# Optimization experiments

Measured on AMD Instinct MI355X. Metric: run time of the kernel, lower is better.

The kernel has to match this reference:

```python
import jax, jax.numpy as jnp
import numpy as np

HEADS = 8
DIM_HEAD = 64

def setup_inputs() -> dict:
    key = jax.random.key(0)
    ks = jax.random.split(key, 5)
    B, n, dim = 128, 512, 256
    inner = HEADS * DIM_HEAD  # 512
    return {
        'x': jax.random.normal(ks[0], (B, n, dim), dtype=jnp.float32),
        'Wq': jax.random.normal(ks[1], (dim, inner), dtype=jnp.float32) * (dim ** -0.5),
        'Wkv': jax.random.normal(ks[2], (dim, 2 * inner), dtype=jnp.float32) * (dim ** -0.5),
        'Wo': jax.random.normal(ks[3], (inner, dim), dtype=jnp.float32) * (inner ** -0.5),
        'bo': jnp.zeros((dim,), dtype=jnp.float32),
        'tie_attn_dim': 64,
    }

def reference(x, Wq, Wkv, Wo, bo, tie_attn_dim):
    h, dh = HEADS, DIM_HEAD
    B, n, dim = x.shape
    r = tie_attn_dim
    b = B // r
    q = x @ Wq                      # [B, n, h*dh]
    kv = x @ Wkv                    # [B, n, 2*h*dh] (self-attention: context = x)
    k, v = jnp.split(kv, 2, axis=-1)
    # '(b r) n (h d) -> b r h n d'
    def to_tied(t):
        return t.reshape(b, r, n, h, dh).transpose(0, 1, 3, 2, 4)
    q, k, v = map(to_tied, (q, k, v))
    scale = (dh ** -0.5) * (r ** -0.5)
    # tied row attention: reduce over MSA rows r and head dim d
    dots = jnp.einsum('brhid,brhjd->bhij', q, k) * scale  # [b, h, n, n]
    attn = jax.nn.softmax(dots, axis=-1)
    out = jnp.einsum('bhij,brhjd->brhid', attn, v)        # [b, r, h, n, dh]
    # 'b r h n d -> (b r) n (h d)'
    out = out.transpose(0, 1, 3, 2, 4).reshape(B, n, h * dh)
    return out @ Wo + bo
```

## Files before the change

kernel.cpp:

```cpp
#include <hip/hip_runtime.h>

typedef unsigned short u16;
typedef __attribute__((ext_vector_type(8))) short bf16x8;
typedef __attribute__((ext_vector_type(4))) float f32x4;

struct __align__(8) U16x4 { u16 a, b, c, d; };

__device__ __forceinline__ u16 f2bf(float f) {
  union { float f; unsigned int u; } cv; cv.f = f;
  unsigned int u = cv.u;
  unsigned int r = (u + 0x7fffu + ((u >> 16) & 1u)) >> 16;
  return (u16)r;
}

__device__ __forceinline__ void gld16(const u16* g, u16* l) {
  __builtin_amdgcn_global_load_lds((const __attribute__((address_space(1))) void*)g,
                                   (__attribute__((address_space(3))) void*)l, 16, 0, 0);
}

__global__ void conv_k(const float* __restrict__ x, u16* __restrict__ xbf) {
  size_t i = ((size_t)blockIdx.x * 256 + threadIdx.x) * 8;
  u16 tmp[8];
  #pragma unroll
  for (int j = 0; j < 8; j++) tmp[j] = f2bf(x[i + j]);
  *(bf16x8*)&xbf[i] = *(const bf16x8*)&tmp[0];
}

__global__ void prep_k(const float* __restrict__ Wq, const float* __restrict__ Wkv,
                       const float* __restrict__ Wo, u16* __restrict__ WT1,
                       u16* __restrict__ WoT) {
  int idx = blockIdx.x * 256 + threadIdx.x;
  if (idx < 1536 * 256) {
    int c = idx >> 8, k = idx & 255;
    WT1[idx] = (c < 512) ? f2bf(Wq[(size_t)k * 512 + c])
                         : f2bf(Wkv[(size_t)k * 1024 + (c - 512)]);
  }
  if (idx < 256 * 512) {
    int nn = idx >> 9, kk = idx & 511;
    WoT[idx] = f2bf(Wo[(size_t)kk * 256 + nn]);
  }
}

template<int KIND>
__global__ void __launch_bounds__(256, 2) gemm_k(
    const u16* __restrict__ A, const u16* __restrict__ B,
    u16* __restrict__ C, u16* __restrict__ C2,
    float* __restrict__ SF, const float* __restrict__ bias, int nkRt) {
  __shared__ __align__(16) u16 lA[128 * 32];
  __shared__ __align__(16) u16 lB[128 * 32];

  const int tid  = threadIdx.x;
  const int bid  = blockIdx.x;
  const int lane = tid & 63;
  const int wv   = tid >> 6;
  const int l15  = lane & 15;
  const int quad = lane >> 4;
  const int mq   = (wv & 1) * 64;
  const int nq   = (wv >> 1) * 64;

  int m0, n0, NK, kb0 = 0;
  int r4 = 0, i0 = 0, s = 0, p = 0;
  if constexpr (KIND == 1) {
    m0 = (bid % 256) * 128; n0 = (bid / 256) * 128; NK = 8;
  } else if constexpr (KIND == 2) {
    n0 = (bid & 3) * 128; m0 = ((bid >> 2) & 3) * 128;
    p = (bid >> 4) & 7; s = bid >> 7; NK = nkRt; kb0 = s * nkRt;
  } else if constexpr (KIND == 3) {
    n0 = (bid & 31) * 128; m0 = ((bid >> 5) & 3) * 128; p = bid >> 7; NK = 16;
  } else {
    n0 = (bid & 1) * 128; m0 = (bid >> 1) * 128; NK = 16;
    r4 = (m0 >> 9) & 63; i0 = m0 & 511;
  }

  f32x4 acc[4][4];
  #pragma unroll
  for (int i = 0; i < 4; i++)
    #pragma unroll
    for (int j = 0; j < 4; j++)
      #pragma unroll
      for (int g = 0; g < 4; g++) acc[i][j][g] = 0.f;

  const int ar0 = tid >> 2;
  const int ac0 = (tid & 3) * 8;

  for (int t = 0; t < NK; t++) {
    const int kb = kb0 + t;
    size_t aBase, bBase; int aRS, bRS;
    if constexpr (KIND == 1) {
      aBase = (size_t)m0 * 256 + kb * 32; aRS = 256;
      bBase = (size_t)n0 * 256 + kb * 32; bRS = 256;
    } else if constexpr (KIND == 2) {
      int r = kb >> 1, dlo = (kb & 1) * 32;
      size_t rowblk = (size_t)r * 512;
      aBase = (rowblk + m0) * 1024 + p * 64 + dlo;        aRS = 1024;
      bBase = (rowblk + n0) * 1024 + 512 + p * 64 + dlo;  bRS = 1024;
    } else if constexpr (KIND == 3) {
      aBase = ((size_t)p * 512 + m0) * 512 + kb * 32;   aRS = 512;
      bBase = ((size_t)p * 4096 + n0) * 512 + kb * 32;  bRS = 512;
    } else {
      int h = kb >> 1, dlo = (kb & 1) * 32;
      aBase = ((size_t)h * 512 + i0) * 4096 + r4 * 64 + dlo; aRS = 4096;
      bBase = (size_t)n0 * 512 + kb * 32; bRS = 512;
    }
    gld16(A + aBase + (size_t)ar0 * aRS + ac0,        &lA[tid * 8]);
    gld16(A + aBase + (size_t)(ar0 + 64) * aRS + ac0, &lA[(tid + 256) * 8]);
    gld16(B + bBase + (size_t)ar0 * bRS + ac0,        &lB[tid * 8]);
    gld16(B + bBase + (size_t)(ar0 + 64) * bRS + ac0, &lB[(tid + 256) * 8]);
    __syncthreads();

    bf16x8 af[4], bfr[4];
    #pragma unroll
    for (int mi = 0; mi < 4; mi++)
      af[mi] = *(const bf16x8*)&lA[(mq + mi * 16 + l15) * 32 + quad * 8];
    #pragma unroll
    for (int ni = 0; ni < 4; ni++)
      bfr[ni] = *(const bf16x8*)&lB[(nq + ni * 16 + l15) * 32 + quad * 8];
    #pragma unroll
    for (int mi = 0; mi < 4; mi++)
      #pragma unroll
      for (int ni = 0; ni < 4; ni++)
        acc[mi][ni] = __builtin_amdgcn_mfma_f32_16x16x32_bf16(af[mi], bfr[ni], acc[mi][ni], 0, 0, 0);
    __syncthreads();
  }

  #pragma unroll
  for (int mi = 0; mi < 4; mi++) {
    #pragma unroll
    for (int ni = 0; ni < 4; ni++) {
      if constexpr (KIND == 1) {
        int cgl = n0 + nq + ni * 16 + l15;
        if (n0 < 1024) {
          #pragma unroll
          for (int g = 0; g < 4; g++) {
            int m = m0 + mq + mi * 16 + quad * 4 + g;
            C[(size_t)m * 1024 + cgl] = f2bf(acc[mi][ni][g]);
          }
        } else {
          int cc = cgl - 1024; int h = cc >> 6, d = cc & 63;
          int r = (m0 >> 9) & 63;
          int j0 = (m0 & 511) + mq + mi * 16 + quad * 4;
          U16x4 pk;
          pk.a = f2bf(acc[mi][ni][0]); pk.b = f2bf(acc[mi][ni][1]);
          pk.c = f2bf(acc[mi][ni][2]); pk.d = f2bf(acc[mi][ni][3]);
          *(U16x4*)&C2[((size_t)h * 4096 + r * 64 + d) * 512 + j0] = pk;
        }
      } else if constexpr (KIND == 2) {
        int gn = n0 + nq + ni * 16 + l15;
        #pragma unroll
        for (int g = 0; g < 4; g++) {
          int gm = m0 + mq + mi * 16 + quad * 4 + g;
          SF[((size_t)(s * 8 + p) * 512 + gm) * 512 + gn] = acc[mi][ni][g];
        }
      } else if constexpr (KIND == 3) {
        int gn = n0 + nq + ni * 16 + l15;
        #pragma unroll
        for (int g = 0; g < 4; g++) {
          int gm = m0 + mq + mi * 16 + quad * 4 + g;
          C[((size_t)p * 512 + gm) * 4096 + gn] = f2bf(acc[mi][ni][g]);
        }
      } else {
        int gn = n0 + nq + ni * 16 + l15;
        float bo_f = bias[gn];
        #pragma unroll
        for (int g = 0; g < 4; g++) {
          int gm = m0 + mq + mi * 16 + quad * 4 + g;
          SF[(size_t)gm * 256 + gn] = acc[mi][ni][g] + bo_f;
        }
      }
    }
  }
}

__global__ void softmax_k(const float* __restrict__ SP, u16* __restrict__ P, int nsplit) {
  int bid = blockIdx.x;
  int p = bid >> 9, i = bid & 511;
  int t = threadIdx.x;
  size_t rowbase = ((size_t)p * 512 + i) * 512;
  float v0 = 0.f, v1 = 0.f;
  for (int ss = 0; ss < nsplit; ss++) {
    size_t off = (size_t)ss * 8 * 512 * 512;
    v0 += SP[off + rowbase + t];
    v1 += SP[off + rowbase + t + 256];
  }
  const float scale = 1.0f / 64.0f;
  v0 *= scale; v1 *= scale;

  int wv = t >> 6, ln = t & 63;
  float m = fmaxf(v0, v1);
  for (int o = 32; o > 0; o >>= 1) m = fmaxf(m, __shfl_down(m, o));
  __shared__ float sred[4];
  if (ln == 0) sred[wv] = m;
  __syncthreads();
  m = fmaxf(fmaxf(sred[0], sred[1]), fmaxf(sred[2], sred[3]));

  float e0 = expf(v0 - m), e1 = expf(v1 - m);
  float sum = e0 + e1;
  for (int o = 32; o > 0; o >>= 1) sum += __shfl_down(sum, o);
  __shared__ float sred2[4];
  if (ln == 0) sred2[wv] = sum;
  __syncthreads();
  float inv = 1.0f / (sred2[0] + sred2[1] + sred2[2] + sred2[3]);

  P[rowbase + t]       = f2bf(e0 * inv);
  P[rowbase + t + 256] = f2bf(e1 * inv);
}

extern "C" void kernel_launch(void* const* d_in, const int* in_sizes, int n_in,
                              void* d_out, int out_size, void* d_ws, size_t ws_size,
                              hipStream_t stream) {
  (void)in_sizes; (void)n_in; (void)out_size;
  const float* x   = (const float*)d_in[0];
  const float* Wq  = (const float*)d_in[1];
  const float* Wkv = (const float*)d_in[2];
  const float* Wo  = (const float*)d_in[3];
  const float* bo  = (const float*)d_in[4];
  float* out = (float*)d_out;

  char* ws = (char*)d_ws;
  size_t off = 0;
  u16* WT1 = (u16*)(ws + off); off += (size_t)1536 * 256 * 2;
  u16* WoT = (u16*)(ws + off); off += (size_t)256 * 512 * 2;
  u16* QKb = (u16*)(ws + off); off += (size_t)32768 * 1024 * 2;
  u16* OTb = QKb;
  u16* VTb = (u16*)(ws + off); off += (size_t)8 * 4096 * 512 * 2;
  u16* Pb  = (u16*)(ws + off); off += (size_t)8 * 512 * 512 * 2;
  char* XS = ws + off;
  u16* xbf = (u16*)XS;
  float* SPb = (float*)XS;
  size_t rem = (ws_size > off) ? (ws_size - off) : 0;
  int nsplit = 4;
  while (nsplit > 1 && (size_t)nsplit * 8 * 512 * 512 * 4 > rem) nsplit >>= 1;

  prep_k<<<dim3(1536), dim3(256), 0, stream>>>(Wq, Wkv, Wo, WT1, WoT);

  for (int bt = 0; bt < 2; bt++) {
    const float* xb = x + (size_t)bt * 32768 * 256;
    float* outb = out + (size_t)bt * 32768 * 256;
    conv_k<<<dim3(4096), dim3(256), 0, stream>>>(xb, xbf);
    gemm_k<1><<<dim3(3072), dim3(256), 0, stream>>>(xbf, WT1, QKb, VTb, nullptr, nullptr, 0);
    gemm_k<2><<<dim3(nsplit * 128), dim3(256), 0, stream>>>(QKb, QKb, nullptr, nullptr,
                                                            SPb, nullptr, 128 / nsplit);
    softmax_k<<<dim3(4096), dim3(256), 0, stream>>>(SPb, Pb, nsplit);
    gemm_k<3><<<dim3(1024), dim3(256), 0, stream>>>(Pb, VTb, OTb, nullptr, nullptr, nullptr, 0);
    gemm_k<4><<<dim3(512), dim3(256), 0, stream>>>(OTb, WoT, nullptr, nullptr, outb, bo, 0);
  }
}
```

Baseline: 407.3 us.

## Stage GEMM epilogues through shared memory for coalesced vectorized global stores

New measurement: 415.4 us. 1.02x slower.

```diff
diff --git a/kernel.cpp b/kernel.cpp
--- a/kernel.cpp
+++ b/kernel.cpp
@@ -46,8 +46,9 @@
     const u16* __restrict__ A, const u16* __restrict__ B,
     u16* __restrict__ C, u16* __restrict__ C2,
     float* __restrict__ SF, const float* __restrict__ bias, int nkRt) {
-  __shared__ __align__(16) u16 lA[128 * 32];
-  __shared__ __align__(16) u16 lB[128 * 32];
+  __shared__ __align__(16) u16 lsm[9216];
+  u16* lA = lsm;
+  u16* lB = lsm + 4096;
 
   const int tid  = threadIdx.x;
   const int bid  = blockIdx.x;
@@ -59,7 +60,7 @@
   const int nq   = (wv >> 1) * 64;
 
   int m0, n0, NK, kb0 = 0;
-  int r4 = 0, i0 = 0, s = 0, p = 0;
+  int s = 0, p = 0;
   if constexpr (KIND == 1) {
     m0 = (bid % 256) * 128; n0 = (bid / 256) * 128; NK = 8;
   } else if constexpr (KIND == 2) {
@@ -69,7 +70,6 @@
     n0 = (bid & 31) * 128; m0 = ((bid >> 5) & 3) * 128; p = bid >> 7; NK = 16;
   } else {
     n0 = (bid & 1) * 128; m0 = (bid >> 1) * 128; NK = 16;
-    r4 = (m0 >> 9) & 63; i0 = m0 & 511;
   }
 
   f32x4 acc[4][4];
@@ -99,7 +99,8 @@
       bBase = ((size_t)p * 4096 + n0) * 512 + kb * 32;  bRS = 512;
     } else {
       int h = kb >> 1, dlo = (kb & 1) * 32;
-      aBase = ((size_t)h * 512 + i0) * 4096 + r4 * 64 + dlo; aRS = 4096;
+      aBase = ((size_t)h * 512 + (m0 & 511)) * 4096 + ((m0 >> 9) & 63) * 64 + dlo;
+      aRS = 4096;
       bBase = (size_t)n0 * 512 + kb * 32; bRS = 512;
     }
     gld16(A + aBase + (size_t)ar0 * aRS + ac0,        &lA[tid * 8]);
@@ -123,50 +124,102 @@
     __syncthreads();
   }
 
-  #pragma unroll
-  for (int mi = 0; mi < 4; mi++) {
-    #pragma unroll
-    for (int ni = 0; ni < 4; ni++) {
-      if constexpr (KIND == 1) {
-        int cgl = n0 + nq + ni * 16 + l15;
-        if (n0 < 1024) {
+  if constexpr (KIND == 1 || KIND == 3) {
+    if (KIND == 3 || n0 < 1024) {
+      #pragma unroll
+      for (int ps = 0; ps < 2; ps++) {
+        if ((mq >> 6) == ps) {
           #pragma unroll
-          for (int g = 0; g < 4; g++) {
-            int m = m0 + mq + mi * 16 + quad * 4 + g;
-            C[(size_t)m * 1024 + cgl] = f2bf(acc[mi][ni][g]);
+          for (int mi = 0; mi < 4; mi++)
+            #pragma unroll
+            for (int ni = 0; ni < 4; ni++) {
+              int lr = mi * 16 + quad * 4;
+              int lc = nq + ni * 16 + l15;
+              #pragma unroll
+              for (int g = 0; g < 4; g++)
+                lsm[(lr + g) * 136 + lc] = f2bf(acc[mi][ni][g]);
+            }
+        }
+        __syncthreads();
+        #pragma unroll
+        for (int it = 0; it < 4; it++) {
+          int idx = tid + it * 256;
+          int lr = idx >> 4, c = (idx & 15) * 8;
+          int gm = m0 + ps * 64 + lr;
+          size_t gaddr;
+          if constexpr (KIND == 1) gaddr = (size_t)gm * 1024 + n0 + c;
+          else                     gaddr = ((size_t)p * 512 + gm) * 4096 + n0 + c;
+          *(bf16x8*)&C[gaddr] = *(const bf16x8*)&lsm[lr * 136 + c];
+        }
+        __syncthreads();
+      }
+    } else {
+      #pragma unroll
+      for (int ps = 0; ps < 2; ps++) {
+        if ((nq >> 6) == ps) {
+          #pragma unroll
+          for (int mi = 0; mi < 4; mi++)
+            #pragma unroll
+            for (int ni = 0; ni < 4; ni++) {
+              int lrn = ni * 16 + l15;
+              int lcm = mq + mi * 16 + quad * 4;
+              U16x4 pk;
+              pk.a = f2bf(acc[mi][ni][0]); pk.b = f2bf(acc[mi][ni][1]);
+              pk.c = f2bf(acc[mi][ni][2]); pk.d = f2bf(acc[mi][ni][3]);
+              *(U16x4*)&lsm[lrn * 136 + lcm] = pk;
+            }
+        }
+        __syncthreads();
+        int r  = (m0 >> 9) & 63;
+        int jb = (m0 & 511);
+        #pragma unroll
+        for (int it = 0; it < 4; it++) {
+          int idx = tid + it * 256;
+          int lr = idx >> 4, c = (idx & 15) * 8;
+          int cc = (n0 - 1024) + ps * 64 + lr;
+          int h = cc >> 6, d = cc & 63;
+          size_t gaddr = ((size_t)h * 4096 + r * 64 + d) * 512 + jb + c;
+          *(bf16x8*)&C2[gaddr] = *(const bf16x8*)&lsm[lr * 136 + c];
+        }
+        __syncthreads();
+      }
+    }
+  } else {
+    float* lsf = (float*)lsm;
+    #pragma unroll
+    for (int ps = 0; ps < 4; ps++) {
+      if ((mq >> 6) == (ps >> 1)) {
+        int miA = (ps & 1) * 2;
+        #pragma unroll
+        for (int mm = 0; mm < 2; mm++) {
+          int mi = miA + mm;
+          #pragma unroll
+          for (int ni = 0; ni < 4; ni++) {
+            int lr = mm * 16 + quad * 4;
+            int lc = nq + ni * 16 + l15;
+            #pragma unroll
+            for (int g = 0; g < 4; g++)
+              lsf[(lr + g) * 132 + lc] = acc[mi][ni][g];
           }
+        }
+      }
+      __syncthreads();
+      #pragma unroll
+      for (int it = 0; it < 4; it++) {
+        int idx = tid + it * 256;
+        int lr = idx >> 5, c = (idx & 31) * 4;
+        int gm = m0 + ps * 32 + lr;
+        f32x4 v = *(const f32x4*)&lsf[lr * 132 + c];
+        if constexpr (KIND == 2) {
+          SF[((size_t)(s * 8 + p) * 512 + gm) * 512 + n0 + c] = v[0],
+          *(f32x4*)&SF[((size_t)(s * 8 + p) * 512 + gm) * 512 + n0 + c] = v;
         } else {
-          int cc = cgl - 1024; int h = cc >> 6, d = cc & 63;
-          int r = (m0 >> 9) & 63;
-          int j0 = (m0 & 511) + mq + mi * 16 + quad * 4;
-          U16x4 pk;
-          pk.a = f2bf(acc[mi][ni][0]); pk.b = f2bf(acc[mi][ni][1]);
-          pk.c = f2bf(acc[mi][ni][2]); pk.d = f2bf(acc[mi][ni][3]);
-          *(U16x4*)&C2[((size_t)h * 4096 + r * 64 + d) * 512 + j0] = pk;
-        }
-      } else if constexpr (KIND == 2) {
-        int gn = n0 + nq + ni * 16 + l15;
-        #pragma unroll
-        for (int g = 0; g < 4; g++) {
-          int gm = m0 + mq + mi * 16 + quad * 4 + g;
-          SF[((size_t)(s * 8 + p) * 512 + gm) * 512 + gn] = acc[mi][ni][g];
-        }
-      } else if constexpr (KIND == 3) {
-        int gn = n0 + nq + ni * 16 + l15;
-        #pragma unroll
-        for (int g = 0; g < 4; g++) {
-          int gm = m0 + mq + mi * 16 + quad * 4 + g;
-          C[((size_t)p * 512 + gm) * 4096 + gn] = f2bf(acc[mi][ni][g]);
-        }
-      } else {
-        int gn = n0 + nq + ni * 16 + l15;
-        float bo_f = bias[gn];
-        #pragma unroll
-        for (int g = 0; g < 4; g++) {
-          int gm = m0 + mq + mi * 16 + quad * 4 + g;
-          SF[(size_t)gm * 256 + gn] = acc[mi][ni][g] + bo_f;
+          f32x4 bo4 = *(const f32x4*)&bias[n0 + c];
+          v[0] += bo4[0]; v[1] += bo4[1]; v[2] += bo4[2]; v[3] += bo4[3];
+          *(f32x4*)&SF[(size_t)gm * 256 + n0 + c] = v;
         }
       }
+      __syncthreads();
     }
   }
 }
```
